# Performance work log

Measured on AMD Instinct MI355X. Metric: run time of the kernel, lower is better.

## Reference

```python
import jax, jax.numpy as jnp
import numpy as np

B, T, V, E, H, NL = 32, 64, 32000, 300, 512, 2
NF, D = 128, 32  # num midi frames, midi_frame_dim
LSTM_IN = E + D  # 332


def setup_inputs() -> dict:
    key = jax.random.key(0)
    ks = jax.random.split(key, 20)
    s = 0.05
    inp = {
        "input_seq": jax.random.randint(ks[0], (B, T), 0, V),
        "midi_sequence": jax.random.normal(ks[1], (B, NF, D), jnp.float32),
        "emb": jax.random.normal(ks[2], (V, E), jnp.float32) * s,
        "mp_w": jax.random.normal(ks[3], (D, D), jnp.float32) * s,
        "mp_b": jnp.zeros((D,), jnp.float32),
        "wh": jax.random.normal(ks[4], (H, H), jnp.float32) * s,
        "wm": jax.random.normal(ks[5], (H, D), jnp.float32) * s,
        "v": jax.random.normal(ks[6], (1, H), jnp.float32) * s,
        "w_ih0": jax.random.normal(ks[7], (4 * H, LSTM_IN), jnp.float32) * s,
        "w_hh0": jax.random.normal(ks[8], (4 * H, H), jnp.float32) * s,
        "b_ih0": jnp.zeros((4 * H,), jnp.float32),
        "b_hh0": jnp.zeros((4 * H,), jnp.float32),
        "w_ih1": jax.random.normal(ks[9], (4 * H, H), jnp.float32) * s,
        "w_hh1": jax.random.normal(ks[10], (4 * H, H), jnp.float32) * s,
        "b_ih1": jnp.zeros((4 * H,), jnp.float32),
        "b_hh1": jnp.zeros((4 * H,), jnp.float32),
        "fc_w": jax.random.uniform(ks[11], (V, H), jnp.float32, -0.1, 0.1),
        "fc_b": jnp.zeros((V,), jnp.float32),
    }
    return inp


def _lstm_cell(x, hp, cp, wih, whh, bih, bhh):
    # PyTorch gate order: i, f, g, o
    g = x @ wih.T + hp @ whh.T + bih + bhh
    i, f, gg, o = jnp.split(g, 4, axis=-1)
    cn = jax.nn.sigmoid(f) * cp + jax.nn.sigmoid(i) * jnp.tanh(gg)
    hn = jax.nn.sigmoid(o) * jnp.tanh(cn)
    return hn, cn


def reference(input_seq, midi_sequence, emb, mp_w, mp_b, wh, wm, v,
              w_ih0, w_hh0, b_ih0, b_hh0, w_ih1, w_hh1, b_ih1, b_hh1,
              fc_w, fc_b):
    embeddings = emb[input_seq]  # [B,T,E] (dropout = identity in eval)
    midi_proj = jax.nn.relu(jnp.einsum('bfd,ed->bfe', midi_sequence, mp_w) + mp_b)  # [B,NF,D]
    midi_key = jnp.einsum('bfd,hd->bfh', midi_proj, wm)  # precomputed W_m(midi_proj)

    h0 = jnp.zeros((NL, B, H), embeddings.dtype)
    c0 = jnp.zeros((NL, B, H), embeddings.dtype)

    def step(carry, x_t):
        h, c = carry
        h_top = h[-1]  # [B,H]
        energy = jnp.tanh((h_top @ wh.T)[:, None, :] + midi_key)  # [B,NF,H]
        scores = jnp.einsum('bfh,h->bf', energy, v[0])
        attn = jax.nn.softmax(scores, axis=-1)  # [B,NF]
        ctx = jnp.einsum('bf,bfd->bd', attn, midi_proj)  # [B,D]
        x = jnp.concatenate([x_t, ctx], axis=-1)  # [B,E+D]
        h1, c1 = _lstm_cell(x, h[0], c[0], w_ih0, w_hh0, b_ih0, b_hh0)
        h2, c2 = _lstm_cell(h1, h[1], c[1], w_ih1, w_hh1, b_ih1, b_hh1)
        return (jnp.stack([h1, h2]), jnp.stack([c1, c2])), (h2, attn)

    (hF, cF), (outs, attns) = jax.lax.scan(step, (h0, c0), embeddings.transpose(1, 0, 2))
    lstm_out = outs.transpose(1, 0, 2)  # [B,T,H]
    logits = lstm_out @ fc_w.T + fc_b  # [B,T,V]
    return logits, (hF, cF), attns.transpose(1, 0, 2)
```

## Files before the change

kernel.cpp:

```cpp
#include <hip/hip_runtime.h>
#include <hip/hip_bf16.h>

#define Bsz 32
#define Tn  64
#define Vn  32000
#define En  300
#define Hn  512
#define NFn 128
#define Dn  32
#define G4  2048
#define LIN 332
#define NWG 256

#define OFF_MPROJ 0
#define OFF_E0    (OFF_MPROJ + 131072)
#define OFF_PG0B  (OFF_E0 + 4194304)
#define OFF_H1T   (OFF_PG0B + 65536)
#define OFF_H2T0  (OFF_H1T + 16384)
#define OFF_H2T1  (OFF_H2T0 + 16384)
#define OFF_H2BB  (OFF_H2T1 + 16384)
#define OFF_C1T   (OFF_H2BB + 16384)
#define OFF_C2T   (OFF_C1T + 16384)
#define OFF_FLG   (OFF_C2T + 16384)
#define OFF_DONE  (OFF_FLG + 4096)
#define OFF_VC    (OFF_DONE + 256)
#define OFF_MKEY  (OFF_VC + 16)
#define OFF_WHT   (OFF_MKEY + 2097152)
#define OFF_WCTX  (OFF_WHT + 262144)
#define OFF_X     (OFF_WCTX + 65536)
#define OFF_W0    (OFF_X + 655360)
#define OFF_HBF   OFF_X
#define OFF_FCWBF (OFF_X + 524288)

#define O_H1S  0
#define O_H2S  1048576
#define O_QS   2113536
#define O_CTXP 3162112
#define O_DENP 3686400
#define O_ES   3702784

#define OUT_HF  65536000
#define OUT_CF  65568768
#define OUT_ATT 65601536

#define L_HS2   0
#define L_HS1   4096
#define L_GL    8192
#define L_PG0   8480
#define L_C1    8736
#define L_C2    8800
#define L_CTX   8864
#define L_DEN   9128
#define L_QL    9136
#define L_VL    9664
#define L_SP    10192
#define L_ESL   10464
#define L_CP    10480
#define L_W0    11024
#define L_MK    27408
#define L_WH    35856
#define SCAN_LDS_FLOATS 39952
#define SCAN_LDS_BYTES  (SCAN_LDS_FLOATS*4)

typedef __attribute__((ext_vector_type(8))) short short8;
typedef __attribute__((ext_vector_type(4))) float f32x4;
typedef unsigned short u16;

__device__ __forceinline__ float frcp(float x){ return __builtin_amdgcn_rcpf(x); }
__device__ __forceinline__ float ftanh(float x){
  float e = __expf(2.0f*x);
  return 1.0f - 2.0f*frcp(e+1.0f);
}
__device__ __forceinline__ float fsig(float x){
  return frcp(1.0f + __expf(-x));
}
__device__ __forceinline__ u16 f2bf(float f){
  __hip_bfloat16 h = __float2bfloat16(f);
  u16 r; __builtin_memcpy(&r, &h, 2); return r;
}

__device__ __forceinline__ float ldc1(const float* p){
  return __hip_atomic_load(p, __ATOMIC_RELAXED, __HIP_MEMORY_SCOPE_AGENT);
}
__device__ __forceinline__ void stc1(float* p, float v){
  __hip_atomic_store(p, v, __ATOMIC_RELAXED, __HIP_MEMORY_SCOPE_AGENT);
}

__device__ __forceinline__ void flag_store(float* ws, int c, int slot, float v){
  stc1(ws + OFF_FLG + c*256 + slot*4, v);
}
__device__ __forceinline__ void waitA(float* ws, int c, float tgt, int tid){
  __syncthreads();
  if (tid < 64){
    const float* fl = ws + OFF_FLG + c*256;
    unsigned cc = 0;
    while (true){
      float v = ldc1(fl + tid*4);
      if (__ballot(v >= tgt) == ~0ull) break;
      if (++cc >= (1u<<22)) break;
    }
  }
  __syncthreads();
  asm volatile("" ::: "memory");
}

__device__ __forceinline__ float redux32(float (&v)[32], int L){
  #pragma unroll
  for (int i=0;i<5;i++){
    const int m = 1<<i, h = 16>>i;
    const bool up = (L & m);
    #pragma unroll
    for (int u=0; u<h; u++){
      float send = up ? v[u] : v[u+h];
      float keep = up ? v[u+h] : v[u];
      v[u] = keep + __shfl_xor(send, m, 64);
    }
  }
  v[0] += __shfl_xor(v[0], 32, 64);
  return v[0];
}
__device__ __forceinline__ float redux16(float (&v)[16], int L){
  #pragma unroll
  for (int i=0;i<4;i++){
    const int m = 1<<i, h = 8>>i;
    const bool up = (L & m);
    #pragma unroll
    for (int u=0; u<h; u++){
      float send = up ? v[u] : v[u+h];
      float keep = up ? v[u+h] : v[u];
      v[u] = keep + __shfl_xor(send, m, 64);
    }
  }
  v[0] += __shfl_xor(v[0], 16, 64);
  v[0] += __shfl_xor(v[0], 32, 64);
  return v[0];
}

__global__ __launch_bounds__(1024) void p1_midi(
    const float* __restrict__ midi, const float* __restrict__ mp_w,
    const float* __restrict__ mp_b, const float* __restrict__ wm,
    float* __restrict__ ws)
{
  __shared__ float ms[NFn*Dn];
  __shared__ float pj[NFn*33];
  __shared__ float mpw[Dn*33];
  __shared__ float mpb[Dn];
  int b = blockIdx.x, tid = threadIdx.x;
  for (int i=tid;i<NFn*Dn;i+=1024) ms[i] = midi[b*NFn*Dn + i];
  { int e = tid>>5, d = tid&31; mpw[e*33+d] = mp_w[tid]; }
  if (tid < Dn) mpb[tid] = mp_b[tid];
  __syncthreads();
  float* mproj = ws + OFF_MPROJ;
  for (int i=tid;i<NFn*Dn;i+=1024){
    int f = i>>5, e = i&31;
    float a = mpb[e];
    #pragma unroll
    for (int d=0;d<Dn;d++) a += ms[f*32+d]*mpw[e*33+d];
    a = fmaxf(a, 0.0f);
    pj[f*33+e] = a;
    mproj[b*NFn*Dn + i] = a;
  }
  __syncthreads();
  int h = tid & 511, fh = tid >> 9;
  float wreg[32];
  #pragma unroll
  for (int d=0;d<32;d++) wreg[d] = wm[h*32+d];
  float* mkf = ws + OFF_MKEY + b*(NFn*Hn);
  for (int ff=0; ff<64; ff++){
    int f = fh*64 + ff;
    float a = 0.f;
    #pragma unroll
    for (int d=0;d<32;d++) a += pj[f*33+d]*wreg[d];
    mkf[f*512 + h] = a;
  }
}

__global__ __launch_bounds__(256) void p2a_x(
    const int* __restrict__ seq, const float* __restrict__ emb,
    float* __restrict__ ws)
{
  int idx = blockIdx.x*256 + threadIdx.x;
  int bt = idx / 80, c4 = idx - bt*80;
  int b = bt & 31, t = bt >> 5;
  float4 x = {0.f,0.f,0.f,0.f};
  if (c4 < 75){
    int s = seq[b*Tn + t];
    x = *(const float4*)(emb + (long)s*En + c4*4);
  }
  *(float4*)(ws + OFF_X + bt*320 + c4*4) = x;
}

__global__ __launch_bounds__(256) void p2b_w(
    const float* __restrict__ wih0, float* __restrict__ ws)
{
  int idx = blockIdx.x*256 + threadIdx.x;
  int j = idx / 80, c4 = idx - j*80;
  float4 x = {0.f,0.f,0.f,0.f};
  if (c4 < 75) x = *(const float4*)(wih0 + (long)j*LIN + c4*4);
  *(float4*)(ws + OFF_W0 + j*320 + c4*4) = x;
}

__global__ __launch_bounds__(256) void p2c_e0(
    const float* __restrict__ ws_c, const float* __restrict__ bih0,
    const float* __restrict__ bhh0, float* __restrict__ ws)
{
  const float* A  = ws_c + OFF_W0;
  const float* Bm = ws_c + OFF_X;
  __shared__ float Al[32][132];
  __shared__ float Bl[32][132];
  int tid = threadIdx.x;
  int j0t = blockIdx.x*128, bt0 = blockIdx.y*128;
  int tx = tid & 15, ty = tid >> 4;
  float acc[8][8];
  #pragma unroll
  for (int i=0;i<8;i++)
    #pragma unroll
    for (int j=0;j<8;j++) acc[i][j] = 0.f;

  int m = tid >> 1;
  int kq = (tid & 1) * 16;
  for (int kk=0; kk<320; kk+=32){
    __syncthreads();
    {
      const float* As = A  + (long)(j0t+m)*320 + kk + kq;
      const float* Bs = Bm + (long)(bt0+m)*320 + kk + kq;
      float4 a0 = *(const float4*)(As+0), a1 = *(const float4*)(As+4);
      float4 a2 = *(const float4*)(As+8), a3 = *(const float4*)(As+12);
      float4 b0 = *(const float4*)(Bs+0), b1 = *(const float4*)(Bs+4);
      float4 b2 = *(const float4*)(Bs+8), b3 = *(const float4*)(Bs+12);
      Al[kq+0][m]=a0.x; Al[kq+1][m]=a0.y; Al[kq+2][m]=a0.z; Al[kq+3][m]=a0.w;
      Al[kq+4][m]=a1.x; Al[kq+5][m]=a1.y; Al[kq+6][m]=a1.z; Al[kq+7][m]=a1.w;
      Al[kq+8][m]=a2.x; Al[kq+9][m]=a2.y; Al[kq+10][m]=a2.z; Al[kq+11][m]=a2.w;
      Al[kq+12][m]=a3.x; Al[kq+13][m]=a3.y; Al[kq+14][m]=a3.z; Al[kq+15][m]=a3.w;
      Bl[kq+0][m]=b0.x; Bl[kq+1][m]=b0.y; Bl[kq+2][m]=b0.z; Bl[kq+3][m]=b0.w;
      Bl[kq+4][m]=b1.x; Bl[kq+5][m]=b1.y; Bl[kq+6][m]=b1.z; Bl[kq+7][m]=b1.w;
      Bl[kq+8][m]=b2.x; Bl[kq+9][m]=b2.y; Bl[kq+10][m]=b2.z; Bl[kq+11][m]=b2.w;
      Bl[kq+12][m]=b3.x; Bl[kq+13][m]=b3.y; Bl[kq+14][m]=b3.z; Bl[kq+15][m]=b3.w;
    }
    __syncthreads();
    #pragma unroll 4
    for (int k=0;k<32;k++){
      float4 a0 = *(const float4*)&Al[k][ty*8];
      float4 a1 = *(const float4*)&Al[k][ty*8+4];
      float4 b0 = *(const float4*)&Bl[k][tx*8];
      float4 b1 = *(const float4*)&Bl[k][tx*8+4];
      float av[8] = {a0.x,a0.y,a0.z,a0.w,a1.x,a1.y,a1.z,a1.w};
      float bv[8] = {b0.x,b0.y,b0.z,b0.w,b1.x,b1.y,b1.z,b1.w};
      #pragma unroll
      for (int i=0;i<8;i++)
        #pragma unroll
        for (int j=0;j<8;j++) acc[i][j] += av[i]*bv[j];
    }
  }
  float* E0 = ws + OFF_E0;
  #pragma unroll
  for (int i=0;i<8;i++){
    int j = j0t + ty*8 + i;
    float be = bih0[j] + bhh0[j];
    #pragma unroll
    for (int jj=0;jj<8;jj++){
      int c = bt0 + tx*8 + jj;
      int tt = c >> 5, bb = c & 31;
      E0[tt*65536 + (bb>>3)*16384 + j*8 + (bb&7)] = acc[i][jj] + be;
    }
  }
}

__global__ __launch_bounds__(256) void p3_cvt(
    const float* __restrict__ fcw, float* __restrict__ ws)
{
  u16* dst = (u16*)(ws + OFF_FCWBF);
  int base = (blockIdx.x*256 + threadIdx.x)*8;
  float4 x = *(const float4*)(fcw+base);
  float4 y = *(const float4*)(fcw+base+4);
  short8 p;
  p[0]=(short)f2bf(x.x); p[1]=(short)f2bf(x.y); p[2]=(short)f2bf(x.z); p[3]=(short)f2bf(x.w);
  p[4]=(short)f2bf(y.x); p[5]=(short)f2bf(y.y); p[6]=(short)f2bf(y.z); p[7]=(short)f2bf(y.w);
  *(short8*)(dst+base) = p;
}

__global__ __launch_bounds__(256) void p5_wctx(
    const float* __restrict__ wih0, float* __restrict__ ws)
{
  int idx = blockIdx.x*256 + threadIdx.x;
  int j = idx >> 5, d = idx & 31;
  ws[OFF_WCTX + idx] = wih0[(long)j*LIN + En + d];
}

__global__ __launch_bounds__(512) void p6_vc(
    const float* __restrict__ v, float* __restrict__ ws)
{
  __shared__ float s[8];
  int tid = threadIdx.x;
  float a = fabsf(v[tid]);
  #pragma unroll
  for (int m=1;m<64;m<<=1) a += __shfl_xor(a, m, 64);
  if ((tid&63)==0) s[tid>>6] = a;
  __syncthreads();
  if (tid==0){
    float c=0;
    #pragma unroll
    for (int i=0;i<8;i++) c += s[i];
    ws[OFF_VC] = c;
  }
}

__global__ __launch_bounds__(256) void p0_init(float* __restrict__ ws,
                                               float* __restrict__ out){
  int idx = blockIdx.x*256 + threadIdx.x;
  out[O_H2S + idx] = 0.f;
  if (idx < 4352) ws[OFF_FLG + idx] = 0.f;
}

__global__ __launch_bounds__(256, 1)
void scan_all(
    const float* __restrict__ wih1, const float* __restrict__ whh1,
    const float* __restrict__ whh0, const float* __restrict__ bih1,
    const float* __restrict__ bhh1, const float* __restrict__ wh,
    const float* __restrict__ vvec, float* __restrict__ ws,
    float* __restrict__ out)
{
  extern __shared__ float lds[];
  float* hs2  = lds + L_HS2;
  float* hs1  = lds + L_HS1;
  float* gl   = lds + L_GL;
  float* pg0l = lds + L_PG0;
  float* c1l  = lds + L_C1;
  float* c2l  = lds + L_C2;
  float* ctxl = lds + L_CTX;
  float* denl = lds + L_DEN;
  float* ql   = lds + L_QL;
  float* vl   = lds + L_VL;
  float* sp   = lds + L_SP;
  float* esl  = lds + L_ESL;
  float* cp   = lds + L_CP;
  float* w0l  = lds + L_W0;
  float* mkl  = lds + L_MK;
  float* whl  = lds + L_WH;

  const int wg = blockIdx.x, tid = threadIdx.x;
  const int rg = wg & 63, bg = wg >> 6;
  const int b2 = wg >> 3, fs = wg & 7;
  const int wv = tid >> 6, L = tid & 63;
  u16* hbf = (u16*)(ws + OFF_HBF);

  const int C_H2 = 0*4+bg, C_Q = 1*4+bg, C_CTX = 2*4+bg, C_H1 = 3*4+bg;

  float w_a[8][8], w_b[8][8];
  #pragma unroll
  for (int r=0;r<8;r++){
    int row = wv*512 + rg*8 + r;
    #pragma unroll
    for (int j=0;j<8;j++){
      w_a[r][j] = wih1[(long)row*512 + j*64 + L];
      w_b[r][j] = whh1[(long)row*512 + j*64 + L];
    }
  }
  for (int c=0; c<64; c++){
    int idx = c*256 + tid;
    int lr = idx >> 9, k = idx & 511;
    int grow = (lr>>3)*512 + rg*8 + (lr&7);
    w0l[idx] = whh0[(long)grow*512 + k];
  }
  for (int c=0; c<32; c++){
    int idx = c*256 + tid;
    int f = idx >> 9, r = idx & 511;
    mkl[f*528 + (r>>5)*33 + (r&31)] =
        ws[OFF_MKEY + b2*65536 + (fs*16+f)*512 + r];
  }
  for (int c=0; c<16; c++){
    int idx = c*256 + tid;
    whl[idx] = wh[(long)(rg*8)*512 + idx];
  }

  const int s4 = ((L&1)<<3) | ((L&2)<<1) | ((L&4)>>1) | ((L&8)>>3);
  const int q_sr = s4 >> 3, q_sx = s4 & 7;
  const int s5 = ((L&1)<<4) | ((L&2)<<2) | (L&4) | ((L&8)>>2) | ((L&16)>>4);
  const int r_sr = s5 >> 3, r_sx = s5 & 7;
  float bsum[2]; int glIdx[2], pgIdx[2];
  #pragma unroll
  for (int p=0;p<2;p++){
    int kk = p*4 + r_sr;
    int row = wv*512 + rg*8 + kk;
    bsum[p] = bih1[row] + bhh1[row];
    glIdx[p] = (wv*8 + kk)*9 + r_sx;
    pgIdx[p] = (wv*8 + kk)*8 + r_sx;
  }

  if (tid < 64){ c1l[tid] = 0.f; c2l[tid] = 0.f; }
  {
    int r = tid>>3, bb = tid&7;
    int row = ((r>>3)<<9) + rg*8 + (r&7);
    pg0l[r*8+bb] = ws[OFF_E0 + bg*16384 + row*8 + bb];
  }
  vl[tid + (tid>>5)] = vvec[tid];
  { int t2 = tid + 256; vl[t2 + (t2>>5)] = vvec[t2]; }
  const float Cv = ws[OFF_VC];
  __syncthreads();

  for (int t=0; t<64; t++){
    const float tgt = (float)(t+1);
    if (t > 0) waitA(ws, C_H2, (float)t, tid);
    {
      const float* h2b = out + O_H2S + t*16384 + bg*4096;
      float4 v0 = *(const float4*)(h2b +    0 + tid*4);
      float4 v1 = *(const float4*)(h2b + 1024 + tid*4);
      float4 v2 = *(const float4*)(h2b + 2048 + tid*4);
      float4 v3 = *(const float4*)(h2b + 3072 + tid*4);
      int kb = tid >> 1, bb0 = (tid&1)*4;
      hs2[(bb0+0)*512 +   0 + kb] = v0.x; hs2[(bb0+1)*512 +   0 + kb] = v0.y;
      hs2[(bb0+2)*512 +   0 + kb] = v0.z; hs2[(bb0+3)*512 +   0 + kb] = v0.w;
      hs2[(bb0+0)*512 + 128 + kb] = v1.x; hs2[(bb0+1)*512 + 128 + kb] = v1.y;
      hs2[(bb0+2)*512 + 128 + kb] = v1.z; hs2[(bb0+3)*512 + 128 + kb] = v1.w;
      hs2[(bb0+0)*512 + 256 + kb] = v2.x; hs2[(bb0+1)*512 + 256 + kb] = v2.y;
      hs2[(bb0+2)*512 + 256 + kb] = v2.z; hs2[(bb0+3)*512 + 256 + kb] = v2.w;
      hs2[(bb0+0)*512 + 384 + kb] = v3.x; hs2[(bb0+1)*512 + 384 + kb] = v3.y;
      hs2[(bb0+2)*512 + 384 + kb] = v3.z; hs2[(bb0+3)*512 + 384 + kb] = v3.w;
    }
    __syncthreads();
    {
      const float* w0p = whl + (wv*2)*512;
      const float* w1p = w0p + 512;
      float vq[16];
      #pragma unroll
      for (int i=0;i<16;i++) vq[i] = 0.f;
      #pragma unroll
      for (int j=0;j<8;j++){
        int k = j*64 + L;
        float wa = w0p[k], wb = w1p[k];
        #pragma unroll
        for (int x=0;x<8;x++){
          float hv = hs2[x*512+k];
          vq[x] += wa*hv; vq[8+x] += wb*hv;
        }
      }
      float qv = redux16(vq, L);
      if (L < 16)
        stc1(out + O_QS + t*16384 + (bg*8+q_sx)*512 + rg*8 + wv*2 + q_sr, qv);
    }
    __syncthreads();
    if (tid == 0) flag_store(ws, C_Q, rg, tgt);

    waitA(ws, C_Q, tgt, tid);
    ql[tid + (tid>>5)] = out[O_QS + t*16384 + b2*512 + tid];
    { int t2 = tid + 256; ql[t2 + (t2>>5)] = out[O_QS + t*16384 + b2*512 + t2]; }
    __syncthreads();
    {
      int f = tid>>4, hg = tid&15;
      const float* mkr = mkl + f*528 + hg*33;
      const float* qb = ql + hg*33;
      const float* vb = vl + hg*33;
      float s = 0.f;
      #pragma unroll
      for (int c=0; c<32; c+=4){
        float4 m4 = *(const float4*)(mkr+c);
        s += vb[c+0]*ftanh(qb[c+0]+m4.x) + vb[c+1]*ftanh(qb[c+1]+m4.y)
           + vb[c+2]*ftanh(qb[c+2]+m4.z) + vb[c+3]*ftanh(qb[c+3]+m4.w);
      }
      sp[f*17+hg] = s;
    }
    __syncthreads();
    if (tid < 16){
      float s = 0.f;
      #pragma unroll
      for (int g=0; g<16; g++) s += sp[tid*17+g];
      float e = __expf(s - Cv);
      esl[tid] = e;
      stc1(out + O_ES + t*4096 + b2*128 + fs*16 + tid, e);
    }
    __syncthreads();
    if (tid == 0){
      float d = 0.f;
      #pragma unroll
      for (int i=0;i<16;i++) d += esl[i];
      stc1(out + O_DENP + t*256 + b2*8 + fs, d);
    }
    {
      int d2 = tid&31, f0 = tid>>5;
      cp[d2*17+f0]   = esl[f0]  * ws[OFF_MPROJ + b2*4096 + (fs*16+f0)*32   + d2];
      cp[d2*17+f0+8] = esl[f0+8]* ws[OFF_MPROJ + b2*4096 + (fs*16+f0+8)*32 + d2];
    }
    __syncthreads();
    if (tid < 32){
      float s = 0.f;
      #pragma unroll
      for (int ff=0; ff<16; ff++) s += cp[tid*17+ff];
      stc1(out + O_CTXP + t*8192 + b2*256 + fs*32 + tid, s);
    }
    __syncthreads();
    if (tid == 0) flag_store(ws, C_CTX, rg, tgt);

    waitA(ws, C_CTX, tgt, tid);
    if (tid < 8){
      float dsum = 0.f;
      #pragma unroll
      for (int f2=0; f2<8; f2++) dsum += out[O_DENP + t*256 + (bg*8+tid)*8 + f2];
      denl[tid] = frcp(dsum);
    }
    __syncthreads();
    {
      int bb = tid>>5, d = tid&31;
      float s = 0.f;
      #pragma unroll
      for (int f2=0; f2<8; f2++) s += out[O_CTXP + t*8192 + (bg*8+bb)*256 + f2*32 + d];
      ctxl[bb*33+d] = s * denl[bb];
    }
    if (rg == 0){
      #pragma unroll
      for (int i0=0; i0<4; i0++){
        int i = tid + i0*256;
        int bb = i>>7, f = i&127;
        float e = out[O_ES + t*4096 + (bg*8+bb)*128 + f];
        __builtin_nontemporal_store(e * denl[bb],
            out + OUT_ATT + (bg*8+bb)*8192 + t*128 + f);
      }
    }
    __syncthreads();
    {
      int r = tid>>3, bb = tid&7;
      int row = ((r>>3)<<9) + rg*8 + (r&7);
      float g0 = pg0l[r*8+bb];
      const float* wr = ws + OFF_WCTX + row*32;
      #pragma unroll
      for (int d2=0; d2<32; d2+=4){
        float4 w4 = *(const float4*)(wr+d2);
        g0 += w4.x*ctxl[bb*33+d2] + w4.y*ctxl[bb*33+d2+1]
            + w4.z*ctxl[bb*33+d2+2] + w4.w*ctxl[bb*33+d2+3];
      }
      gl[r*9+bb] = g0;
    }
    __syncthreads();
    if (tid < 64){
      int kk = tid>>3, bb = tid&7;
      float gi = gl[(kk)*9+bb],     gf = gl[(8+kk)*9+bb];
      float gg2 = gl[(16+kk)*9+bb], go = gl[(24+kk)*9+bb];
      float cp2 = c1l[tid];
      float cn = fsig(gf)*cp2 + fsig(gi)*ftanh(gg2);
      float hn = fsig(go)*ftanh(cn);
      c1l[tid] = cn;
      stc1(out + O_H1S + t*16384 + bg*4096 + (rg*8+kk)*8 + bb, hn);
      if (t == 63){
        int bgl = bg*8+bb, kgl = rg*8+kk;
        __builtin_nontemporal_store(hn, out + OUT_HF + bgl*512 + kgl);
        __builtin_nontemporal_store(cn, out + OUT_CF + bgl*512 + kgl);
      }
    }
    __syncthreads();
    if (tid == 0) flag_store(ws, C_H1, rg, tgt);

    waitA(ws, C_H1, tgt, tid);
    {
      const float* h1b = out + O_H1S + t*16384 + bg*4096;
      float4 v0 = *(const float4*)(h1b +    0 + tid*4);
      float4 v1 = *(const float4*)(h1b + 1024 + tid*4);
      float4 v2 = *(const float4*)(h1b + 2048 + tid*4);
      float4 v3 = *(const float4*)(h1b + 3072 + tid*4);
      int kb = tid >> 1, bb0 = (tid&1)*4;
      hs1[(bb0+0)*512 +   0 + kb] = v0.x; hs1[(bb0+1)*512 +   0 + kb] = v0.y;
      hs1[(bb0+2)*512 +   0 + kb] = v0.z; hs1[(bb0+3)*512 +   0 + kb] = v0.w;
      hs1[(bb0+0)*512 + 128 + kb] = v1.x; hs1[(bb0+1)*512 + 128 + kb] = v1.y;
      hs1[(bb0+2)*512 + 128 + kb] = v1.z; hs1[(bb0+3)*512 + 128 + kb] = v1.w;
      hs1[(bb0+0)*512 + 256 + kb] = v2.x; hs1[(bb0+1)*512 + 256 + kb] = v2.y;
      hs1[(bb0+2)*512 + 256 + kb] = v2.z; hs1[(bb0+3)*512 + 256 + kb] = v2.w;
      hs1[(bb0+0)*512 + 384 + kb] = v3.x; hs1[(bb0+1)*512 + 384 + kb] = v3.y;
      hs1[(bb0+2)*512 + 384 + kb] = v3.z; hs1[(bb0+3)*512 + 384 + kb] = v3.w;
    }
    __syncthreads();
    #pragma unroll
    for (int p=0; p<2; p++){
      float vals[32];
      #pragma unroll
      for (int i=0;i<32;i++) vals[i] = 0.f;
      #pragma unroll
      for (int j=0;j<8;j++){
        int k = j*64 + L;
        float h1v[8], h2v[8];
        #pragma unroll
        for (int x=0;x<8;x++){ h1v[x] = hs1[x*512+k]; h2v[x] = hs2[x*512+k]; }
        #pragma unroll
        for (int r=0;r<4;r++){
          const float wa = w_a[p*4+r][j], wb = w_b[p*4+r][j];
          #pragma unroll
          for (int x=0;x<8;x++) vals[r*8+x] += wa*h1v[x] + wb*h2v[x];
        }
      }
      float v0 = redux32(vals, L);
      if (L < 32) gl[glIdx[p]] = v0 + bsum[p];
    }
    __syncthreads();
    if (tid < 64){
      int kk = tid>>3, bb = tid&7;
      float gi = gl[(kk)*9+bb],     gf = gl[(8+kk)*9+bb];
      float gg2 = gl[(16+kk)*9+bb], go = gl[(24+kk)*9+bb];
      float cp3 = c2l[tid];
      float cn = fsig(gf)*cp3 + fsig(gi)*ftanh(gg2);
      float hn = fsig(go)*ftanh(cn);
      c2l[tid] = cn;
      int k2 = rg*8+kk, b = bg*8+bb;
      stc1(out + O_H2S + (t+1)*16384 + bg*4096 + k2*8 + bb, hn);
      __builtin_nontemporal_store(f2bf(hn), hbf + (t*32+b)*512 + k2);
      if (t == 63){
        __builtin_nontemporal_store(hn, out + OUT_HF + 16384 + b*512 + k2);
        __builtin_nontemporal_store(cn, out + OUT_CF + 16384 + b*512 + k2);
      }
    }
    __syncthreads();
    if (tid == 0) flag_store(ws, C_H2, rg, tgt);

    if (t < 63){
      #pragma unroll
      for (int p=0; p<2; p++){
        float vals[32];
        #pragma unroll
        for (int i=0;i<32;i++) vals[i] = 0.f;
        #pragma unroll
        for (int j=0;j<8;j++){
          int k = j*64 + L;
          float h1v[8];
          #pragma unroll
          for (int x=0;x<8;x++) h1v[x] = hs1[x*512+k];
          #pragma unroll
          for (int r=0;r<4;r++){
            const float wc = w0l[(wv*8 + p*4 + r)*512 + k];
            #pragma unroll
            for (int x=0;x<8;x++) vals[r*8+x] += wc*h1v[x];
          }
        }
        float v0 = redux32(vals, L);
        if (L < 32) pg0l[pgIdx[p]] = v0;
      }
      __syncthreads();
      {
        int r = tid>>3, bb = tid&7;
        int row = ((r>>3)<<9) + rg*8 + (r&7);
        pg0l[r*8+bb] += __builtin_nontemporal_load(
            ws + OFF_E0 + (t+1)*65536 + bg*16384 + row*8 + bb);
      }
    }
  }
}

__global__ __launch_bounds__(256) void fc_gemm(
    const float* __restrict__ ws_f, const float* __restrict__ fcb,
    float* __restrict__ out)
{
  const u16* A  = (const u16*)(ws_f + OFF_FCWBF);
  const u16* Bm = (const u16*)(ws_f + OFF_HBF);
  __shared__ u16 Al[128*40];
  __shared__ u16 Bl[128*40];
  int tid = threadIdx.x;
  int v0 = blockIdx.x*128, bt0 = blockIdx.y*128;
  int lane = tid & 63, wv = tid >> 6;
  int wr = wv >> 1, wc = wv & 1;
  f32x4 acc[4][4];
  #pragma unroll
  for (int i=0;i<4;i++)
    #pragma unroll
    for (int j=0;j<4;j++) acc[i][j] = (f32x4){0.f,0.f,0.f,0.f};

  int ar = wr*64 + (lane&15);
  int br = wc*64 + (lane&15);
  int ks = (lane>>4)*8;

  for (int kk=0; kk<512; kk+=32){
    __syncthreads();
    #pragma unroll
    for (int i=0;i<2;i++){
      int ld = tid + 256*i;
      int row = ld >> 2, cs = (ld & 3)*8;
      *(int4*)(&Al[row*40+cs]) = *(const int4*)(A  + (v0+row)*512 + kk + cs);
      *(int4*)(&Bl[row*40+cs]) = *(const int4*)(Bm + (bt0+row)*512 + kk + cs);
    }
    __syncthreads();
    short8 af[4], bf[4];
    #pragma unroll
    for (int m=0;m<4;m++) af[m] = *(const short8*)(&Al[(ar+m*16)*40 + ks]);
    #pragma unroll
    for (int n=0;n<4;n++) bf[n] = *(const short8*)(&Bl[(br+n*16)*40 + ks]);
    #pragma unroll
    for (int m=0;m<4;m++)
      #pragma unroll
      for (int n=0;n<4;n++)
        acc[m][n] = __builtin_amdgcn_mfma_f32_16x16x32_bf16(af[m], bf[n], acc[m][n], 0,0,0);
  }
  int r4 = (lane>>4)*4;
  #pragma unroll
  for (int m=0;m<4;m++){
    int v = v0 + wr*64 + m*16 + r4;
    float4 bias = *(const float4*)(fcb + v);
    #pragma unroll
    for (int n=0;n<4;n++){
      int bt = bt0 + wc*64 + n*16 + (lane&15);
      int b = bt & 31, t = bt >> 5;
      f32x4 a = acc[m][n];
      float4 res = { a[0]+bias.x, a[1]+bias.y, a[2]+bias.z, a[3]+bias.w };
      *(float4*)(out + b*2048000 + t*32000 + v) = res;
    }
  }
}

extern "C" void kernel_launch(void* const* d_in, const int* in_sizes, int n_in,
                              void* d_out, int out_size, void* d_ws, size_t ws_size,
                              hipStream_t stream)
{
  const int*   seq  = (const int*)d_in[0];
  const float* midi = (const float*)d_in[1];
  const float* emb  = (const float*)d_in[2];
  const float* mpw  = (const float*)d_in[3];
  const float* mpb  = (const float*)d_in[4];
  const float* wh   = (const float*)d_in[5];
  const float* wm   = (const float*)d_in[6];
  const float* vv   = (const float*)d_in[7];
  const float* wih0 = (const float*)d_in[8];
  const float* whh0 = (const float*)d_in[9];
  const float* bih0 = (const float*)d_in[10];
  const float* bhh0 = (const float*)d_in[11];
  const float* wih1 = (const float*)d_in[12];
  const float* whh1 = (const float*)d_in[13];
  const float* bih1 = (const float*)d_in[14];
  const float* bhh1 = (const float*)d_in[15];
  const float* fcw  = (const float*)d_in[16];
  const float* fcb  = (const float*)d_in[17];
  float* out = (float*)d_out;
  float* ws  = (float*)d_ws;

  hipFuncSetAttribute((const void*)scan_all,
                      hipFuncAttributeMaxDynamicSharedMemorySize,
                      SCAN_LDS_BYTES);

  p1_midi<<<32, 1024, 0, stream>>>(midi, mpw, mpb, wm, ws);
  p2a_x  <<<640, 256, 0, stream>>>(seq, emb, ws);
  p2b_w  <<<640, 256, 0, stream>>>(wih0, ws);
  p2c_e0 <<<dim3(16,16), 256, 0, stream>>>(ws, bih0, bhh0, ws);
  p3_cvt <<<8000, 256, 0, stream>>>(fcw, ws);
  p5_wctx<<<256, 256, 0, stream>>>(wih0, ws);
  p6_vc  <<<1, 512, 0, stream>>>(vv, ws);
  p0_init<<<64, 256, 0, stream>>>(ws, out);

  scan_all<<<NWG, 256, SCAN_LDS_BYTES, stream>>>(wih1, whh1, whh0, bih1, bhh1,
                                                 wh, vv, ws, out);

  fc_gemm<<<dim3(250,16), 256, 0, stream>>>(ws, fcb, out);
}
```

Measured before the change: 5.542 ms.

## Double scan workgroup size to 512 threads, halving per-thread work

The persistent recurrent scan kernel now runs 512 threads per workgroup instead of 256. Each wave owns 4 gate rows instead of 8, so register-resident weights, LDS fills, the query projection, the attention score partials and the layer-0 recurrent matvec are all split across twice as many waves. The aim is to shorten the latency-bound per-step critical path with more parallelism and fewer registers per thread. In exchange it adds more threads per barrier, some idle threads in the tid<256 sections, and a slightly larger LDS layout for the score partial buffer.

Result: faster. 4.960 ms (-10.5%).

```diff
diff --git a/kernel.cpp b/kernel.cpp
--- a/kernel.cpp
+++ b/kernel.cpp
@@ -54,12 +54,12 @@
 #define L_QL    9136
 #define L_VL    9664
 #define L_SP    10192
-#define L_ESL   10464
-#define L_CP    10480
-#define L_W0    11024
-#define L_MK    27408
-#define L_WH    35856
-#define SCAN_LDS_FLOATS 39952
+#define L_ESL   10720
+#define L_CP    10736
+#define L_W0    11280
+#define L_MK    27664
+#define L_WH    36112
+#define SCAN_LDS_FLOATS 40208
 #define SCAN_LDS_BYTES  (SCAN_LDS_FLOATS*4)
 
 typedef __attribute__((ext_vector_type(8))) short short8;
@@ -119,10 +119,10 @@
   v[0] += __shfl_xor(v[0], 32, 64);
   return v[0];
 }
-__device__ __forceinline__ float redux16(float (&v)[16], int L){
-  #pragma unroll
-  for (int i=0;i<4;i++){
-    const int m = 1<<i, h = 8>>i;
+__device__ __forceinline__ float redux8(float (&v)[8], int L){
+  #pragma unroll
+  for (int i=0;i<3;i++){
+    const int m = 1<<i, h = 4>>i;
     const bool up = (L & m);
     #pragma unroll
     for (int u=0; u<h; u++){
@@ -131,6 +131,7 @@
       v[u] = keep + __shfl_xor(send, m, 64);
     }
   }
+  v[0] += __shfl_xor(v[0], 8, 64);
   v[0] += __shfl_xor(v[0], 16, 64);
   v[0] += __shfl_xor(v[0], 32, 64);
   return v[0];
@@ -312,7 +313,7 @@
   if (idx < 4352) ws[OFF_FLG + idx] = 0.f;
 }
 
-__global__ __launch_bounds__(256, 1)
+__global__ __launch_bounds__(512, 1)
 void scan_all(
     const float* __restrict__ wih1, const float* __restrict__ whh1,
     const float* __restrict__ whh0, const float* __restrict__ bih1,
@@ -341,60 +342,55 @@
   const int wg = blockIdx.x, tid = threadIdx.x;
   const int rg = wg & 63, bg = wg >> 6;
   const int b2 = wg >> 3, fs = wg & 7;
-  const int wv = tid >> 6, L = tid & 63;
+  const int W = tid >> 6, L = tid & 63;
   u16* hbf = (u16*)(ws + OFF_HBF);
 
   const int C_H2 = 0*4+bg, C_Q = 1*4+bg, C_CTX = 2*4+bg, C_H1 = 3*4+bg;
 
-  float w_a[8][8], w_b[8][8];
-  #pragma unroll
-  for (int r=0;r<8;r++){
-    int row = wv*512 + rg*8 + r;
+  float w_a[4][8], w_b[4][8];
+  #pragma unroll
+  for (int r=0;r<4;r++){
+    int lr = W*4 + r;
+    int row = ((lr>>3)<<9) + rg*8 + (lr&7);
     #pragma unroll
     for (int j=0;j<8;j++){
       w_a[r][j] = wih1[(long)row*512 + j*64 + L];
       w_b[r][j] = whh1[(long)row*512 + j*64 + L];
     }
   }
-  for (int c=0; c<64; c++){
-    int idx = c*256 + tid;
+  for (int c=0; c<32; c++){
+    int idx = c*512 + tid;
     int lr = idx >> 9, k = idx & 511;
     int grow = (lr>>3)*512 + rg*8 + (lr&7);
     w0l[idx] = whh0[(long)grow*512 + k];
   }
-  for (int c=0; c<32; c++){
-    int idx = c*256 + tid;
+  for (int c=0; c<16; c++){
+    int idx = c*512 + tid;
     int f = idx >> 9, r = idx & 511;
     mkl[f*528 + (r>>5)*33 + (r&31)] =
         ws[OFF_MKEY + b2*65536 + (fs*16+f)*512 + r];
   }
-  for (int c=0; c<16; c++){
-    int idx = c*256 + tid;
+  for (int c=0; c<8; c++){
+    int idx = c*512 + tid;
     whl[idx] = wh[(long)(rg*8)*512 + idx];
   }
 
-  const int s4 = ((L&1)<<3) | ((L&2)<<1) | ((L&4)>>1) | ((L&8)>>3);
-  const int q_sr = s4 >> 3, q_sx = s4 & 7;
   const int s5 = ((L&1)<<4) | ((L&2)<<2) | (L&4) | ((L&8)>>2) | ((L&16)>>4);
   const int r_sr = s5 >> 3, r_sx = s5 & 7;
-  float bsum[2]; int glIdx[2], pgIdx[2];
-  #pragma unroll
-  for (int p=0;p<2;p++){
-    int kk = p*4 + r_sr;
-    int row = wv*512 + rg*8 + kk;
-    bsum[p] = bih1[row] + bhh1[row];
-    glIdx[p] = (wv*8 + kk)*9 + r_sx;
-    pgIdx[p] = (wv*8 + kk)*8 + r_sx;
-  }
+  const int lr_g = W*4 + r_sr;
+  const int row_g = ((lr_g>>3)<<9) + rg*8 + (lr_g&7);
+  const float bsum = bih1[row_g] + bhh1[row_g];
+  const int glIdx = lr_g*9 + r_sx;
+  const int pgIdx = lr_g*8 + r_sx;
+  const int brev = ((L&1)<<2) | (L&2) | ((L>>2)&1);
 
   if (tid < 64){ c1l[tid] = 0.f; c2l[tid] = 0.f; }
-  {
+  if (tid < 256){
     int r = tid>>3, bb = tid&7;
     int row = ((r>>3)<<9) + rg*8 + (r&7);
     pg0l[r*8+bb] = ws[OFF_E0 + bg*16384 + row*8 + bb];
   }
   vl[tid + (tid>>5)] = vvec[tid];
-  { int t2 = tid + 256; vl[t2 + (t2>>5)] = vvec[t2]; }
   const float Cv = ws[OFF_VC];
   __syncthreads();
 
@@ -403,67 +399,58 @@
     if (t > 0) waitA(ws, C_H2, (float)t, tid);
     {
       const float* h2b = out + O_H2S + t*16384 + bg*4096;
-      float4 v0 = *(const float4*)(h2b +    0 + tid*4);
-      float4 v1 = *(const float4*)(h2b + 1024 + tid*4);
-      float4 v2 = *(const float4*)(h2b + 2048 + tid*4);
-      float4 v3 = *(const float4*)(h2b + 3072 + tid*4);
-      int kb = tid >> 1, bb0 = (tid&1)*4;
-      hs2[(bb0+0)*512 +   0 + kb] = v0.x; hs2[(bb0+1)*512 +   0 + kb] = v0.y;
-      hs2[(bb0+2)*512 +   0 + kb] = v0.z; hs2[(bb0+3)*512 +   0 + kb] = v0.w;
-      hs2[(bb0+0)*512 + 128 + kb] = v1.x; hs2[(bb0+1)*512 + 128 + kb] = v1.y;
-      hs2[(bb0+2)*512 + 128 + kb] = v1.z; hs2[(bb0+3)*512 + 128 + kb] = v1.w;
-      hs2[(bb0+0)*512 + 256 + kb] = v2.x; hs2[(bb0+1)*512 + 256 + kb] = v2.y;
-      hs2[(bb0+2)*512 + 256 + kb] = v2.z; hs2[(bb0+3)*512 + 256 + kb] = v2.w;
-      hs2[(bb0+0)*512 + 384 + kb] = v3.x; hs2[(bb0+1)*512 + 384 + kb] = v3.y;
-      hs2[(bb0+2)*512 + 384 + kb] = v3.z; hs2[(bb0+3)*512 + 384 + kb] = v3.w;
+      #pragma unroll
+      for (int c=0;c<2;c++){
+        int i = c*512 + tid;
+        float4 v = *(const float4*)(h2b + i*4);
+        int k = i>>1, bb0 = (i&1)*4;
+        hs2[(bb0+0)*512+k]=v.x; hs2[(bb0+1)*512+k]=v.y;
+        hs2[(bb0+2)*512+k]=v.z; hs2[(bb0+3)*512+k]=v.w;
+      }
     }
     __syncthreads();
     {
-      const float* w0p = whl + (wv*2)*512;
-      const float* w1p = w0p + 512;
-      float vq[16];
-      #pragma unroll
-      for (int i=0;i<16;i++) vq[i] = 0.f;
+      const float* w0p = whl + W*512;
+      float vq[8];
+      #pragma unroll
+      for (int i=0;i<8;i++) vq[i] = 0.f;
       #pragma unroll
       for (int j=0;j<8;j++){
         int k = j*64 + L;
-        float wa = w0p[k], wb = w1p[k];
+        float wa = w0p[k];
         #pragma unroll
-        for (int x=0;x<8;x++){
-          float hv = hs2[x*512+k];
-          vq[x] += wa*hv; vq[8+x] += wb*hv;
-        }
-      }
-      float qv = redux16(vq, L);
-      if (L < 16)
-        stc1(out + O_QS + t*16384 + (bg*8+q_sx)*512 + rg*8 + wv*2 + q_sr, qv);
+        for (int x=0;x<8;x++) vq[x] += wa*hs2[x*512+k];
+      }
+      float qv = redux8(vq, L);
+      if (L < 8)
+        stc1(out + O_QS + t*16384 + (bg*8+brev)*512 + rg*8 + W, qv);
     }
     __syncthreads();
     if (tid == 0) flag_store(ws, C_Q, rg, tgt);
 
     waitA(ws, C_Q, tgt, tid);
     ql[tid + (tid>>5)] = out[O_QS + t*16384 + b2*512 + tid];
-    { int t2 = tid + 256; ql[t2 + (t2>>5)] = out[O_QS + t*16384 + b2*512 + t2]; }
     __syncthreads();
     {
-      int f = tid>>4, hg = tid&15;
-      const float* mkr = mkl + f*528 + hg*33;
-      const float* qb = ql + hg*33;
-      const float* vb = vl + hg*33;
+      int f = tid>>5, hg = tid&31;
+      int base = (hg>>1)*33 + (hg&1)*16;
+      const float* mkr = mkl + f*528 + base;
+      const float* qb = ql + base;
+      const float* vb = vl + base;
       float s = 0.f;
       #pragma unroll
-      for (int c=0; c<32; c+=4){
+      for (int c=0; c<16; c+=4){
         float4 m4 = *(const float4*)(mkr+c);
         s += vb[c+0]*ftanh(qb[c+0]+m4.x) + vb[c+1]*ftanh(qb[c+1]+m4.y)
            + vb[c+2]*ftanh(qb[c+2]+m4.z) + vb[c+3]*ftanh(qb[c+3]+m4.w);
       }
-      sp[f*17+hg] = s;
+      sp[f*33+hg] = s;
     }
     __syncthreads();
     if (tid < 16){
       float s = 0.f;
       #pragma unroll
-      for (int g=0; g<16; g++) s += sp[tid*17+g];
+      for (int g=0; g<32; g++) s += sp[tid*33+g];
       float e = __expf(s - Cv);
       esl[tid] = e;
       stc1(out + O_ES + t*4096 + b2*128 + fs*16 + tid, e);
@@ -477,8 +464,7 @@
     }
     {
       int d2 = tid&31, f0 = tid>>5;
-      cp[d2*17+f0]   = esl[f0]  * ws[OFF_MPROJ + b2*4096 + (fs*16+f0)*32   + d2];
-      cp[d2*17+f0+8] = esl[f0+8]* ws[OFF_MPROJ + b2*4096 + (fs*16+f0+8)*32 + d2];
+      cp[d2*17+f0] = esl[f0] * ws[OFF_MPROJ + b2*4096 + (fs*16+f0)*32 + d2];
     }
     __syncthreads();
     if (tid < 32){
@@ -498,7 +484,7 @@
       denl[tid] = frcp(dsum);
     }
     __syncthreads();
-    {
+    if (tid < 256){
       int bb = tid>>5, d = tid&31;
       float s = 0.f;
       #pragma unroll
@@ -507,8 +493,8 @@
     }
     if (rg == 0){
       #pragma unroll
-      for (int i0=0; i0<4; i0++){
-        int i = tid + i0*256;
+      for (int i0=0; i0<2; i0++){
+        int i = tid + i0*512;
         int bb = i>>7, f = i&127;
         float e = out[O_ES + t*4096 + (bg*8+bb)*128 + f];
         __builtin_nontemporal_store(e * denl[bb],
@@ -516,7 +502,7 @@
       }
     }
     __syncthreads();
-    {
+    if (tid < 256){
       int r = tid>>3, bb = tid&7;
       int row = ((r>>3)<<9) + rg*8 + (r&7);
       float g0 = pg0l[r*8+bb];
@@ -551,23 +537,17 @@
     waitA(ws, C_H1, tgt, tid);
     {
       const float* h1b = out + O_H1S + t*16384 + bg*4096;
-      float4 v0 = *(const float4*)(h1b +    0 + tid*4);
-      float4 v1 = *(const float4*)(h1b + 1024 + tid*4);
-      float4 v2 = *(const float4*)(h1b + 2048 + tid*4);
-      float4 v3 = *(const float4*)(h1b + 3072 + tid*4);
-      int kb = tid >> 1, bb0 = (tid&1)*4;
-      hs1[(bb0+0)*512 +   0 + kb] = v0.x; hs1[(bb0+1)*512 +   0 + kb] = v0.y;
-      hs1[(bb0+2)*512 +   0 + kb] = v0.z; hs1[(bb0+3)*512 +   0 + kb] = v0.w;
-      hs1[(bb0+0)*512 + 128 + kb] = v1.x; hs1[(bb0+1)*512 + 128 + kb] = v1.y;
-      hs1[(bb0+2)*512 + 128 + kb] = v1.z; hs1[(bb0+3)*512 + 128 + kb] = v1.w;
-      hs1[(bb0+0)*512 + 256 + kb] = v2.x; hs1[(bb0+1)*512 + 256 + kb] = v2.y;
-      hs1[(bb0+2)*512 + 256 + kb] = v2.z; hs1[(bb0+3)*512 + 256 + kb] = v2.w;
-      hs1[(bb0+0)*512 + 384 + kb] = v3.x; hs1[(bb0+1)*512 + 384 + kb] = v3.y;
-      hs1[(bb0+2)*512 + 384 + kb] = v3.z; hs1[(bb0+3)*512 + 384 + kb] = v3.w;
-    }
-    __syncthreads();
-    #pragma unroll
-    for (int p=0; p<2; p++){
+      #pragma unroll
+      for (int c=0;c<2;c++){
+        int i = c*512 + tid;
+        float4 v = *(const float4*)(h1b + i*4);
+        int k = i>>1, bb0 = (i&1)*4;
+        hs1[(bb0+0)*512+k]=v.x; hs1[(bb0+1)*512+k]=v.y;
+        hs1[(bb0+2)*512+k]=v.z; hs1[(bb0+3)*512+k]=v.w;
+      }
+    }
+    __syncthreads();
+    {
       float vals[32];
       #pragma unroll
       for (int i=0;i<32;i++) vals[i] = 0.f;
@@ -579,13 +559,13 @@
         for (int x=0;x<8;x++){ h1v[x] = hs1[x*512+k]; h2v[x] = hs2[x*512+k]; }
         #pragma unroll
         for (int r=0;r<4;r++){
-          const float wa = w_a[p*4+r][j], wb = w_b[p*4+r][j];
+          const float wa = w_a[r][j], wb = w_b[r][j];
           #pragma unroll
           for (int x=0;x<8;x++) vals[r*8+x] += wa*h1v[x] + wb*h2v[x];
         }
       }
       float v0 = redux32(vals, L);
-      if (L < 32) gl[glIdx[p]] = v0 + bsum[p];
+      if (L < 32) gl[glIdx] = v0 + bsum;
     }
     __syncthreads();
     if (tid < 64){
@@ -608,8 +588,7 @@
     if (tid == 0) flag_store(ws, C_H2, rg, tgt);
 
     if (t < 63){
-      #pragma unroll
-      for (int p=0; p<2; p++){
+      {
         float vals[32];
         #pragma unroll
         for (int i=0;i<32;i++) vals[i] = 0.f;
@@ -621,16 +600,16 @@
           for (int x=0;x<8;x++) h1v[x] = hs1[x*512+k];
           #pragma unroll
           for (int r=0;r<4;r++){
-            const float wc = w0l[(wv*8 + p*4 + r)*512 + k];
+            const float wc = w0l[(W*4 + r)*512 + k];
             #pragma unroll
             for (int x=0;x<8;x++) vals[r*8+x] += wc*h1v[x];
           }
         }
         float v0 = redux32(vals, L);
-        if (L < 32) pg0l[pgIdx[p]] = v0;
+        if (L < 32) pg0l[pgIdx] = v0;
       }
       __syncthreads();
-      {
+      if (tid < 256){
         int r = tid>>3, bb = tid&7;
         int row = ((r>>3)<<9) + rg*8 + (r&7);
         pg0l[r*8+bb] += __builtin_nontemporal_load(
@@ -737,7 +716,7 @@
   p6_vc  <<<1, 512, 0, stream>>>(vv, ws);
   p0_init<<<64, 256, 0, stream>>>(ws, out);
 
-  scan_all<<<NWG, 256, SCAN_LDS_BYTES, stream>>>(wih1, whh1, whh0, bih1, bhh1,
+  scan_all<<<NWG, 512, SCAN_LDS_BYTES, stream>>>(wih1, whh1, whh0, bih1, bhh1,
                                                  wh, vv, ws, out);
 
   fc_gemm<<<dim3(250,16), 256, 0, stream>>>(ws, fcb, out);
```
